# Kernel optimization log

Measured on AMD Instinct MI355X. Metric: run time of the kernel, lower is better.

## Reference

```python
import jax, jax.numpy as jnp
import numpy as np

NUM_NODES = 100000
FEAT_DIM = 256
H1 = 256
H2 = 256
NUM_CLASSES = 64
B = 4096
F1 = 25
F2 = 10


def setup_inputs() -> dict:
    key = jax.random.key(0)
    k0, k1, k2, ke, kw1, kw2, kw3 = jax.random.split(key, 7)
    T0 = jax.random.randint(k0, (B,), 0, NUM_NODES)
    T1 = jax.random.randint(k1, (B, F1), 0, NUM_NODES)
    T2 = jax.random.randint(k2, (B * F1, F2), 0, NUM_NODES)
    emb = jax.random.normal(ke, (NUM_NODES, FEAT_DIM), dtype=jnp.float32)
    # nn.Linear(in, out, bias=False) stores weight as [out, in]
    W1 = jax.random.normal(kw1, (H1, 2 * FEAT_DIM), dtype=jnp.float32) * (1.0 / np.sqrt(2 * FEAT_DIM))
    W2 = jax.random.normal(kw2, (H2, 2 * H1), dtype=jnp.float32) * (1.0 / np.sqrt(2 * H1))
    W3 = jax.random.normal(kw3, (NUM_CLASSES, H2), dtype=jnp.float32) * (1.0 / np.sqrt(H2))
    return {"T0": T0, "T1": T1, "T2": T2, "emb": emb, "W1": W1, "W2": W2, "W3": W3}


def reference(T0, T1, T2, emb, W1, W2, W3):
    # hop-0 roots: [B, D]; hop-1 neighbor mean: [B, D]
    feat_0 = emb[T0]
    x = emb[T1].mean(axis=1)
    h0 = jax.nn.relu(jnp.concatenate([feat_0, x], axis=1) @ W1.T)  # [B, H1]
    # dropout is identity in eval mode (p applied only in training)
    # hop-1 nodes with hop-2 neighbor mean: [B*F1, D] each
    feat_1 = emb[T1].reshape(-1, FEAT_DIM)
    x2 = emb[T2].mean(axis=1)  # [B*F1, D]
    h1 = jax.nn.relu(jnp.concatenate([feat_1, x2], axis=1) @ W1.T)  # [B*F1, H1]
    h1 = h1.reshape(B, F1, H1).mean(axis=1)  # [B, H1]
    combined = jnp.concatenate([h0, h1], axis=1)  # [B, 2*H1]
    embedding = jax.nn.relu(combined @ W2.T)  # [B, H2]
    scores = embedding @ W3.T  # [B, C]
    return scores
```

## Files before the change

kernel.cpp:

```cpp
#include <hip/hip_runtime.h>
#include <hip/hip_bf16.h>


typedef __bf16  bf16x8 __attribute__((ext_vector_type(8)));
typedef __bf16  bf16x4 __attribute__((ext_vector_type(4)));
typedef float   f32x4  __attribute__((ext_vector_type(4)));
typedef float   f32x2  __attribute__((ext_vector_type(2)));

#define BATCH     4096
#define F1        25
#define F2        10
#define NNODES    100000
#define ZY_NT     3125
#define ZY_BLOCKS 512

__device__ __forceinline__ uint2 pack4_bf16(float a, float b, float c, float d) {
    union { __bf16 h[4]; uint2 u; } p;
    p.h[0] = (__bf16)a; p.h[1] = (__bf16)b; p.h[2] = (__bf16)c; p.h[3] = (__bf16)d;
    return p.u;
}

__device__ __forceinline__ f32x2 pkmax0(f32x2 v) {
    f32x2 r; r[0] = fmaxf(v[0], 0.f); r[1] = fmaxf(v[1], 0.f); return r;
}

__global__ __launch_bounds__(256) void prep_weights(const float* __restrict__ W1,
                                                    const float* __restrict__ W2,
                                                    const float* __restrict__ W3,
                                                    __bf16* __restrict__ Wzy,
                                                    __bf16* __restrict__ W2b,
                                                    __bf16* __restrict__ W3b) {
    int blk = blockIdx.x;
    if (blk < 64) {
        int i = blk * 256 + threadIdx.x;
        int r  = i >> 5;
        int c0 = (i & 31) * 8;
        const float* src = (r < 256) ? (W1 + (size_t)r * 512 + c0)
                                     : (W1 + (size_t)(r - 256) * 512 + 256 + c0);
        float4 a = reinterpret_cast<const float4*>(src)[0];
        float4 b = reinterpret_cast<const float4*>(src)[1];
        uint4 o;
        uint2 pa = pack4_bf16(a.x, a.y, a.z, a.w);
        uint2 pb = pack4_bf16(b.x, b.y, b.z, b.w);
        o.x = pa.x; o.y = pa.y; o.z = pb.x; o.w = pb.y;
        *reinterpret_cast<uint4*>(Wzy + (size_t)r * 256 + c0) = o;
    } else {
        const float* in; __bf16* out;
        int i;
        if (blk < 128) { in = W2; out = W2b; i = (blk - 64) * 256 + threadIdx.x; }
        else           { in = W3; out = W3b; i = (blk - 128) * 256 + threadIdx.x; }
        float4 v0 = reinterpret_cast<const float4*>(in)[i * 2];
        float4 v1 = reinterpret_cast<const float4*>(in)[i * 2 + 1];
        uint4 o;
        uint2 a = pack4_bf16(v0.x, v0.y, v0.z, v0.w);
        uint2 b = pack4_bf16(v1.x, v1.y, v1.z, v1.w);
        o.x = a.x; o.y = a.y; o.z = b.x; o.w = b.y;
        reinterpret_cast<uint4*>(out)[i] = o;
    }
}

__global__ __launch_bounds__(512, 2) void gemm_ZY(const float* __restrict__ emb,
                                                  const __bf16* __restrict__ Wzy,
                                                  __bf16* __restrict__ Ztab,
                                                  unsigned char* __restrict__ Y8) {
    __shared__ __align__(16) char Abuf[2][16384];
    __shared__ __align__(16) __bf16 Ybuf[8][32][72];
    const int tid  = threadIdx.x;
    const int wid  = tid >> 6;
    const int lane = tid & 63;
    const int lr   = lane & 15;
    const int kg   = lane >> 4;
    const int n0   = wid * 64;

    bf16x8 wfrag[4][8];
    {
        const __bf16* Wb = Wzy + (size_t)(n0 + lr) * 256 + kg * 8;
#pragma unroll
        for (int ni = 0; ni < 4; ++ni)
#pragma unroll
            for (int kt = 0; kt < 8; ++kt)
                wfrag[ni][kt] = *reinterpret_cast<const bf16x8*>(Wb + ni * 16 * 256 + kt * 32);
    }

    int soff[4];
#pragma unroll
    for (int q = 0; q < 4; ++q) {
        int e  = q * 2048 + tid * 4;
        int r  = e >> 8;
        int cb = (e & 255) * 2;
        soff[q] = r * 512 + (cb ^ ((r & 7) << 4));
    }

    int t = blockIdx.x;
    float4 ld0[4];
    {
        const float4* src = reinterpret_cast<const float4*>(emb + (size_t)t * 8192);
#pragma unroll
        for (int q = 0; q < 4; ++q) ld0[q] = src[q * 512 + tid];
    }
    int cur = 0;

    for (; t < ZY_NT; t += ZY_BLOCKS) {
#pragma unroll
        for (int q = 0; q < 4; ++q) {
            float4 v = ld0[q];
            *reinterpret_cast<uint2*>(Abuf[cur] + soff[q]) = pack4_bf16(v.x, v.y, v.z, v.w);
        }
        int tn = t + ZY_BLOCKS;
        float4 ld1[4] = {};
        if (tn < ZY_NT) {
            const float4* src = reinterpret_cast<const float4*>(emb + (size_t)tn * 8192);
#pragma unroll
            for (int q = 0; q < 4; ++q) ld1[q] = src[q * 512 + tid];
        }
        __syncthreads();

        f32x4 acc[2][4] = {};
        const char* Ab = Abuf[cur];
#pragma unroll
        for (int kt = 0; kt < 8; ++kt) {
            bf16x8 a[2];
#pragma unroll
            for (int mi = 0; mi < 2; ++mi) {
                int r  = mi * 16 + lr;
                int by = kt * 64 + kg * 16;
                a[mi] = *reinterpret_cast<const bf16x8*>(Ab + r * 512 + (by ^ ((r & 7) << 4)));
            }
#pragma unroll
            for (int mi = 0; mi < 2; ++mi)
#pragma unroll
                for (int ni = 0; ni < 4; ++ni)
                    acc[mi][ni] = __builtin_amdgcn_mfma_f32_16x16x32_bf16(a[mi], wfrag[ni][kt], acc[mi][ni], 0, 0, 0);
        }

        const int orow = (lane >> 4) * 4;
        const int ocol = lane & 15;
        const int m0   = t * 32;
#pragma unroll
        for (int mi = 0; mi < 2; ++mi)
#pragma unroll
            for (int ni = 0; ni < 4; ++ni)
#pragma unroll
                for (int j = 0; j < 4; ++j)
                    Ybuf[wid][mi * 16 + orow + j][ni * 16 + ocol] = (__bf16)acc[mi][ni][j];
        const int row = lane & 31;
        const int cg  = (lane >> 5) * 32;
        if (wid < 4) {
#pragma unroll
            for (int q = 0; q < 4; ++q) {
                bf16x8 v = *reinterpret_cast<bf16x8*>(&Ybuf[wid][row][cg + q * 8]);
                *reinterpret_cast<bf16x8*>(Ztab + (size_t)(m0 + row) * 256 + n0 + cg + q * 8) = v;
            }
        } else {
#pragma unroll
            for (int q = 0; q < 4; ++q) {
                bf16x8 v = *reinterpret_cast<bf16x8*>(&Ybuf[wid][row][cg + q * 8]);
                int w0 = 0, w1 = 0;
                w0 = __builtin_amdgcn_cvt_pk_fp8_f32((float)v[0], (float)v[1], w0, false);
                w0 = __builtin_amdgcn_cvt_pk_fp8_f32((float)v[2], (float)v[3], w0, true);
                w1 = __builtin_amdgcn_cvt_pk_fp8_f32((float)v[4], (float)v[5], w1, false);
                w1 = __builtin_amdgcn_cvt_pk_fp8_f32((float)v[6], (float)v[7], w1, true);
                uint2 o; o.x = (unsigned)w0; o.y = (unsigned)w1;
                *reinterpret_cast<uint2*>(Y8 + (size_t)(m0 + row) * 256 + (n0 - 256) + cg + q * 8) = o;
            }
        }

#pragma unroll
        for (int q = 0; q < 4; ++q) ld0[q] = ld1[q];
        cur ^= 1;
    }
}

__global__ __launch_bounds__(256) void agg_kernel(const int* __restrict__ T0,
                                                  const int* __restrict__ T1,
                                                  const int* __restrict__ T2,
                                                  const __bf16* __restrict__ Ztab,
                                                  const unsigned char* __restrict__ Y8,
                                                  __bf16* __restrict__ comb) {
    __shared__ float red1[4][256];
    __shared__ float red0[4][256];
    const int b    = blockIdx.x;
    const int wv   = threadIdx.x >> 6;
    const int lane = threadIdx.x & 63;

    f32x2 m01 = {0.f, 0.f}, m23 = {0.f, 0.f};
    f32x2 g01 = {0.f, 0.f}, g23 = {0.f, 0.f};

    int f = wv;
    {
    }
    int r0  = __builtin_amdgcn_readfirstlane(b * F1 + f);
    int t1c = T1[r0];
    bf16x4   zc  = *reinterpret_cast<const bf16x4*>(Ztab + (size_t)t1c * 256 + lane * 4);
    unsigned y1c = *reinterpret_cast<const unsigned*>(Y8 + (size_t)t1c * 256 + lane * 4);
    unsigned yvc[F2];
#pragma unroll
    for (int j = 0; j < F2; ++j) {
        int ix = T2[(size_t)r0 * F2 + j];
        yvc[j] = *reinterpret_cast<const unsigned*>(Y8 + (size_t)ix * 256 + lane * 4);
    }

    while (true) {
        const int fn = f + 4;
        const bool more = (fn < F1);
        bf16x4 zn; unsigned y1n; unsigned yvn[F2];
        if (more) {
            int rn  = __builtin_amdgcn_readfirstlane(b * F1 + fn);
            int t1n = T1[rn];
            zn  = *reinterpret_cast<const bf16x4*>(Ztab + (size_t)t1n * 256 + lane * 4);
            y1n = *reinterpret_cast<const unsigned*>(Y8 + (size_t)t1n * 256 + lane * 4);
#pragma unroll
            for (int j = 0; j < F2; ++j) {
                int ix = T2[(size_t)rn * F2 + j];
                yvn[j] = *reinterpret_cast<const unsigned*>(Y8 + (size_t)ix * 256 + lane * 4);
            }
        }
        f32x2 s01 = {0.f, 0.f}, s23 = {0.f, 0.f};
#pragma unroll
        for (int j = 0; j < F2; ++j) {
            s01 += __builtin_amdgcn_cvt_pk_f32_fp8(yvc[j], false);
            s23 += __builtin_amdgcn_cvt_pk_f32_fp8(yvc[j], true);
        }
        g01 += __builtin_amdgcn_cvt_pk_f32_fp8(y1c, false);
        g23 += __builtin_amdgcn_cvt_pk_f32_fp8(y1c, true);
        f32x2 z01; z01[0] = (float)zc[0]; z01[1] = (float)zc[1];
        f32x2 z23; z23[0] = (float)zc[2]; z23[1] = (float)zc[3];
        m01 += pkmax0(z01 + s01 * (1.0f / F2));
        m23 += pkmax0(z23 + s23 * (1.0f / F2));
        if (!more) break;
        f = fn; zc = zn; y1c = y1n;
#pragma unroll
        for (int j = 0; j < F2; ++j) yvc[j] = yvn[j];
    }

    {
        float4 t1v; t1v.x = m01[0]; t1v.y = m01[1]; t1v.z = m23[0]; t1v.w = m23[1];
        float4 t0v; t0v.x = g01[0]; t0v.y = g01[1]; t0v.z = g23[0]; t0v.w = g23[1];
        *reinterpret_cast<float4*>(&red1[wv][lane * 4]) = t1v;
        *reinterpret_cast<float4*>(&red0[wv][lane * 4]) = t0v;
    }
    __syncthreads();

    const int col = threadIdx.x;
    float s1 = red1[0][col] + red1[1][col] + red1[2][col] + red1[3][col];
    float s0 = red0[0][col] + red0[1][col] + red0[2][col] + red0[3][col];
    const int t0 = T0[b];
    float z0 = (float)Ztab[(size_t)t0 * 256 + col];
    comb[(size_t)b * 512 + col]       = (__bf16)fmaxf(z0 + s0 * (1.0f / F1), 0.0f);
    comb[(size_t)b * 512 + 256 + col] = (__bf16)(s1 * (1.0f / F1));
}

__global__ __launch_bounds__(256) void gemm_relu_bf16(const __bf16* __restrict__ A,
                                                      const __bf16* __restrict__ W,
                                                      __bf16* __restrict__ C,
                                                      int K, int ldc) {
    int wid  = threadIdx.x >> 6;
    int lane = threadIdx.x & 63;
    int m0 = blockIdx.x * 128 + (wid >> 1) * 64;
    int n0 = blockIdx.y * 128 + (wid & 1) * 64;
    int lr = lane & 15;
    int kg = lane >> 4;

    f32x4 acc[4][4] = {};
    const __bf16* Abase = A + (size_t)(m0 + lr) * K + kg * 8;
    const __bf16* Wbase = W + (size_t)(n0 + lr) * K + kg * 8;

    for (int kt = 0; kt < K; kt += 32) {
        bf16x8 a[4], b[4];
#pragma unroll
        for (int i = 0; i < 4; ++i)
            a[i] = *reinterpret_cast<const bf16x8*>(Abase + (size_t)i * 16 * K + kt);
#pragma unroll
        for (int i = 0; i < 4; ++i)
            b[i] = *reinterpret_cast<const bf16x8*>(Wbase + (size_t)i * 16 * K + kt);
#pragma unroll
        for (int mi = 0; mi < 4; ++mi)
#pragma unroll
            for (int ni = 0; ni < 4; ++ni)
                acc[mi][ni] = __builtin_amdgcn_mfma_f32_16x16x32_bf16(a[mi], b[ni], acc[mi][ni], 0, 0, 0);
    }

    int orow = (lane >> 4) * 4;
    int ocol = lane & 15;
#pragma unroll
    for (int mi = 0; mi < 4; ++mi)
#pragma unroll
        for (int ni = 0; ni < 4; ++ni)
#pragma unroll
            for (int j = 0; j < 4; ++j) {
                float v = fmaxf(acc[mi][ni][j], 0.0f);
                C[(size_t)(m0 + mi * 16 + orow + j) * ldc + (n0 + ni * 16 + ocol)] = (__bf16)v;
            }
}

__global__ __launch_bounds__(256) void gemm_out(const __bf16* __restrict__ A,
                                                const __bf16* __restrict__ W,
                                                float* __restrict__ C) {
    const int K = 256;
    int wid  = threadIdx.x >> 6;
    int lane = threadIdx.x & 63;
    int m0 = blockIdx.x * 128 + wid * 32;
    int lr = lane & 15;
    int kg = lane >> 4;

    f32x4 acc[2][4] = {};
    const __bf16* Abase = A + (size_t)(m0 + lr) * K + kg * 8;
    const __bf16* Wbase = W + (size_t)lr * K + kg * 8;

    for (int kt = 0; kt < K; kt += 32) {
        bf16x8 a[2], b[4];
#pragma unroll
        for (int i = 0; i < 2; ++i)
            a[i] = *reinterpret_cast<const bf16x8*>(Abase + (size_t)i * 16 * K + kt);
#pragma unroll
        for (int i = 0; i < 4; ++i)
            b[i] = *reinterpret_cast<const bf16x8*>(Wbase + (size_t)i * 16 * K + kt);
#pragma unroll
        for (int mi = 0; mi < 2; ++mi)
#pragma unroll
            for (int ni = 0; ni < 4; ++ni)
                acc[mi][ni] = __builtin_amdgcn_mfma_f32_16x16x32_bf16(a[mi], b[ni], acc[mi][ni], 0, 0, 0);
    }

    int orow = (lane >> 4) * 4;
    int ocol = lane & 15;
#pragma unroll
    for (int mi = 0; mi < 2; ++mi)
#pragma unroll
        for (int ni = 0; ni < 4; ++ni)
#pragma unroll
            for (int j = 0; j < 4; ++j)
                C[(size_t)(m0 + mi * 16 + orow + j) * 64 + (ni * 16 + ocol)] = acc[mi][ni][j];
}

extern "C" void kernel_launch(void* const* d_in, const int* in_sizes, int n_in,
                              void* d_out, int out_size, void* d_ws, size_t ws_size,
                              hipStream_t stream) {
    const int*   T0  = (const int*)d_in[0];
    const int*   T1  = (const int*)d_in[1];
    const int*   T2  = (const int*)d_in[2];
    const float* emb = (const float*)d_in[3];
    const float* W1  = (const float*)d_in[4];
    const float* W2  = (const float*)d_in[5];
    const float* W3  = (const float*)d_in[6];
    float* out = (float*)d_out;

    char* ws = (char*)d_ws;
    __bf16*        Wzy  = (__bf16*)(ws);
    __bf16*        W2b  = (__bf16*)(ws + 262144);
    __bf16*        W3b  = (__bf16*)(ws + 524288);
    __bf16*        comb = (__bf16*)(ws + 557056);
    __bf16*        embd = (__bf16*)(ws + 4751360);
    __bf16*        Ztab = (__bf16*)(ws + 6848512);
    unsigned char* Y8   = (unsigned char*)(ws + 58048512);

    prep_weights<<<dim3(136), dim3(256), 0, stream>>>(W1, W2, W3, Wzy, W2b, W3b);

    gemm_ZY<<<dim3(ZY_BLOCKS), dim3(512), 0, stream>>>(emb, Wzy, Ztab, Y8);

    agg_kernel<<<dim3(BATCH), dim3(256), 0, stream>>>(T0, T1, T2, Ztab, Y8, comb);

    gemm_relu_bf16<<<dim3(BATCH / 128, 2), dim3(256), 0, stream>>>(comb, W2b, embd, 512, 256);
    gemm_out<<<dim3(BATCH / 128), dim3(256), 0, stream>>>(embd, W3b, out);
}
```

Measured before the change: 130.8 us.

## Fuse W2 GEMM and output GEMM into one kernel via shared-memory staging

Replaces the separate relu-GEMM with W2 and the final GEMM with W3 by a single kernel. Each 128-row block computes the full 256-wide hidden activation, keeps it in LDS and then multiplies by W3 directly. This removes one launch and the global round-trip of the intermediate embedding. The trade-off is a grid of only 32 blocks with heavy per-thread accumulator state (launch_bounds 256,1), so much of the GPU sits idle and each block does more serial work.

```diff
diff --git a/kernel.cpp b/kernel.cpp
--- a/kernel.cpp
+++ b/kernel.cpp
@@ -187,8 +187,6 @@
     f32x2 g01 = {0.f, 0.f}, g23 = {0.f, 0.f};
 
     int f = wv;
-    {
-    }
     int r0  = __builtin_amdgcn_readfirstlane(b * F1 + f);
     int t1c = T1[r0];
     bf16x4   zc  = *reinterpret_cast<const bf16x4*>(Ztab + (size_t)t1c * 256 + lane * 4);
@@ -250,87 +248,79 @@
     comb[(size_t)b * 512 + 256 + col] = (__bf16)(s1 * (1.0f / F1));
 }
 
-__global__ __launch_bounds__(256) void gemm_relu_bf16(const __bf16* __restrict__ A,
-                                                      const __bf16* __restrict__ W,
-                                                      __bf16* __restrict__ C,
-                                                      int K, int ldc) {
-    int wid  = threadIdx.x >> 6;
-    int lane = threadIdx.x & 63;
-    int m0 = blockIdx.x * 128 + (wid >> 1) * 64;
-    int n0 = blockIdx.y * 128 + (wid & 1) * 64;
-    int lr = lane & 15;
-    int kg = lane >> 4;
-
-    f32x4 acc[4][4] = {};
-    const __bf16* Abase = A + (size_t)(m0 + lr) * K + kg * 8;
-    const __bf16* Wbase = W + (size_t)(n0 + lr) * K + kg * 8;
-
-    for (int kt = 0; kt < K; kt += 32) {
-        bf16x8 a[4], b[4];
-#pragma unroll
-        for (int i = 0; i < 4; ++i)
-            a[i] = *reinterpret_cast<const bf16x8*>(Abase + (size_t)i * 16 * K + kt);
-#pragma unroll
-        for (int i = 0; i < 4; ++i)
-            b[i] = *reinterpret_cast<const bf16x8*>(Wbase + (size_t)i * 16 * K + kt);
+__global__ __launch_bounds__(256, 1) void fused_tail(const __bf16* __restrict__ comb,
+                                                     const __bf16* __restrict__ W2b,
+                                                     const __bf16* __restrict__ W3b,
+                                                     float* __restrict__ out) {
+    __shared__ __bf16 Et[128][264];
+    const int wid  = threadIdx.x >> 6;
+    const int lane = threadIdx.x & 63;
+    const int lr   = lane & 15;
+    const int kg   = lane >> 4;
+    const int gm0  = blockIdx.x * 128;
+
+    {
+        const int m0l = (wid >> 1) * 64;
+        const int n0l = (wid & 1) * 128;
+        f32x4 acc[4][8] = {};
+        const __bf16* Abase = comb + (size_t)(gm0 + m0l + lr) * 512 + kg * 8;
+        const __bf16* Wbase = W2b + (size_t)(n0l + lr) * 512 + kg * 8;
+        for (int kt = 0; kt < 512; kt += 32) {
+            bf16x8 a[4], b[8];
+#pragma unroll
+            for (int i = 0; i < 4; ++i)
+                a[i] = *reinterpret_cast<const bf16x8*>(Abase + (size_t)i * 16 * 512 + kt);
+#pragma unroll
+            for (int i = 0; i < 8; ++i)
+                b[i] = *reinterpret_cast<const bf16x8*>(Wbase + (size_t)i * 16 * 512 + kt);
+#pragma unroll
+            for (int mi = 0; mi < 4; ++mi)
+#pragma unroll
+                for (int ni = 0; ni < 8; ++ni)
+                    acc[mi][ni] = __builtin_amdgcn_mfma_f32_16x16x32_bf16(a[mi], b[ni], acc[mi][ni], 0, 0, 0);
+        }
+        const int orow = (lane >> 4) * 4;
+        const int ocol = lane & 15;
 #pragma unroll
         for (int mi = 0; mi < 4; ++mi)
 #pragma unroll
+            for (int ni = 0; ni < 8; ++ni)
+#pragma unroll
+                for (int j = 0; j < 4; ++j)
+                    Et[m0l + mi * 16 + orow + j][n0l + ni * 16 + ocol] =
+                        (__bf16)fmaxf(acc[mi][ni][j], 0.0f);
+    }
+    __syncthreads();
+
+    {
+        const int rl0 = wid * 32;
+        f32x4 acc[2][4] = {};
+        const __bf16* Wbase = W3b + (size_t)lr * 256 + kg * 8;
+        for (int kt = 0; kt < 256; kt += 32) {
+            bf16x8 a[2], b[4];
+#pragma unroll
+            for (int i = 0; i < 2; ++i)
+                a[i] = *reinterpret_cast<const bf16x8*>(&Et[rl0 + i * 16 + lr][kt + kg * 8]);
+#pragma unroll
+            for (int i = 0; i < 4; ++i)
+                b[i] = *reinterpret_cast<const bf16x8*>(Wbase + (size_t)i * 16 * 256 + kt);
+#pragma unroll
+            for (int mi = 0; mi < 2; ++mi)
+#pragma unroll
+                for (int ni = 0; ni < 4; ++ni)
+                    acc[mi][ni] = __builtin_amdgcn_mfma_f32_16x16x32_bf16(a[mi], b[ni], acc[mi][ni], 0, 0, 0);
+        }
+        const int orow = (lane >> 4) * 4;
+        const int ocol = lane & 15;
+#pragma unroll
+        for (int mi = 0; mi < 2; ++mi)
+#pragma unroll
             for (int ni = 0; ni < 4; ++ni)
-                acc[mi][ni] = __builtin_amdgcn_mfma_f32_16x16x32_bf16(a[mi], b[ni], acc[mi][ni], 0, 0, 0);
-    }
-
-    int orow = (lane >> 4) * 4;
-    int ocol = lane & 15;
-#pragma unroll
-    for (int mi = 0; mi < 4; ++mi)
-#pragma unroll
-        for (int ni = 0; ni < 4; ++ni)
-#pragma unroll
-            for (int j = 0; j < 4; ++j) {
-                float v = fmaxf(acc[mi][ni][j], 0.0f);
-                C[(size_t)(m0 + mi * 16 + orow + j) * ldc + (n0 + ni * 16 + ocol)] = (__bf16)v;
-            }
-}
-
-__global__ __launch_bounds__(256) void gemm_out(const __bf16* __restrict__ A,
-                                                const __bf16* __restrict__ W,
-                                                float* __restrict__ C) {
-    const int K = 256;
-    int wid  = threadIdx.x >> 6;
-    int lane = threadIdx.x & 63;
-    int m0 = blockIdx.x * 128 + wid * 32;
-    int lr = lane & 15;
-    int kg = lane >> 4;
-
-    f32x4 acc[2][4] = {};
-    const __bf16* Abase = A + (size_t)(m0 + lr) * K + kg * 8;
-    const __bf16* Wbase = W + (size_t)lr * K + kg * 8;
-
-    for (int kt = 0; kt < K; kt += 32) {
-        bf16x8 a[2], b[4];
-#pragma unroll
-        for (int i = 0; i < 2; ++i)
-            a[i] = *reinterpret_cast<const bf16x8*>(Abase + (size_t)i * 16 * K + kt);
-#pragma unroll
-        for (int i = 0; i < 4; ++i)
-            b[i] = *reinterpret_cast<const bf16x8*>(Wbase + (size_t)i * 16 * K + kt);
-#pragma unroll
-        for (int mi = 0; mi < 2; ++mi)
-#pragma unroll
-            for (int ni = 0; ni < 4; ++ni)
-                acc[mi][ni] = __builtin_amdgcn_mfma_f32_16x16x32_bf16(a[mi], b[ni], acc[mi][ni], 0, 0, 0);
-    }
-
-    int orow = (lane >> 4) * 4;
-    int ocol = lane & 15;
-#pragma unroll
-    for (int mi = 0; mi < 2; ++mi)
-#pragma unroll
-        for (int ni = 0; ni < 4; ++ni)
-#pragma unroll
-            for (int j = 0; j < 4; ++j)
-                C[(size_t)(m0 + mi * 16 + orow + j) * 64 + (ni * 16 + ocol)] = acc[mi][ni][j];
+#pragma unroll
+                for (int j = 0; j < 4; ++j)
+                    out[(size_t)(gm0 + rl0 + mi * 16 + orow + j) * 64 + (ni * 16 + ocol)] =
+                        acc[mi][ni][j];
+    }
 }
 
 extern "C" void kernel_launch(void* const* d_in, const int* in_sizes, int n_in,
@@ -350,7 +340,6 @@
     __bf16*        W2b  = (__bf16*)(ws + 262144);
     __bf16*        W3b  = (__bf16*)(ws + 524288);
     __bf16*        comb = (__bf16*)(ws + 557056);
-    __bf16*        embd = (__bf16*)(ws + 4751360);
     __bf16*        Ztab = (__bf16*)(ws + 6848512);
     unsigned char* Y8   = (unsigned char*)(ws + 58048512);
 
@@ -360,6 +349,5 @@
 
     agg_kernel<<<dim3(BATCH), dim3(256), 0, stream>>>(T0, T1, T2, Ztab, Y8, comb);
 
-    gemm_relu_bf16<<<dim3(BATCH / 128, 2), dim3(256), 0, stream>>>(comb, W2b, embd, 512, 256);
-    gemm_out<<<dim3(BATCH / 128), dim3(256), 0, stream>>>(embd, W3b, out);
-}
+    fused_tail<<<dim3(BATCH / 128), dim3(256), 0, stream>>>(comb, W2b, W3b, out);
+}
```

New measurement: 138.5 us. 5.8% more time.
